# Performance work log

Hardware: AMD Instinct MI355X
Metric: run time of the kernel (lower is better)

The kernel has to match this reference:

```python
import jax, jax.numpy as jnp
import numpy as np

K = 7
SIGMA = 1.0
NUM_CLASSES = 17


def setup_inputs() -> dict:
    key = jax.random.key(0)
    k1, k2, k3 = jax.random.split(key, 3)
    B, C, N = 4, NUM_CLASSES, 4096
    logits = jax.random.normal(k1, (B, C, N), dtype=jnp.float32)
    labels = jax.random.randint(k2, (B, N), 0, NUM_CLASSES, dtype=jnp.int32)
    ins_T = jax.random.normal(k3, (B * N, NUM_CLASSES, NUM_CLASSES), dtype=jnp.float32)
    return {"logits": logits, "labels": labels, "ins_T": ins_T}


def reference(logits, labels, ins_T):
    B, C, N = logits.shape
    k = K
    x = jnp.transpose(logits, (0, 2, 1))  # [B, N, C]

    # Pairwise squared distances [B, N, N] and (k+1)-NN (smallest dists)
    sq = jnp.sum(x * x, axis=-1)  # [B, N]
    dists = sq[:, :, None] + sq[:, None, :] - 2.0 * jnp.einsum('bnc,bmc->bnm', x, x)
    _, idx = jax.lax.top_k(-dists, k + 1)  # smallest distances first
    idx = idx[:, :, 1:]  # drop self -> [B, N, k]

    flat = x.reshape(B * N, C)                 # [BN, C]
    labf = labels.reshape(-1)                  # [BN]
    idxf = (idx + jnp.arange(B)[:, None, None] * N).reshape(B * N, k)  # [BN, k]

    neigh_logits = flat[idxf]                          # [BN, k, C]
    neigh_labels = labf[idxf]                          # [BN, k]
    neigh_T = ins_T[idxf].reshape(B * N, k, -1)        # [BN, k, C*C]

    # distance map: +1 same label, -1 different, weighted by RBF affinity
    dmap = jnp.where(neigh_labels == labf[:, None], 1.0, -1.0)
    eij = jnp.exp(-jnp.sum((flat[:, None, :] - neigh_logits) ** 2, axis=2)
                  / (2.0 * SIGMA ** 2))
    dmap = jax.lax.stop_gradient(dmap * eij)  # detached in original

    T_dist = jnp.sum((ins_T.reshape(B * N, 1, -1) - neigh_T) ** 2, axis=2)  # [BN, k]
    return jnp.mean(dmap * T_dist)
```

## Files before the change

kernel.cpp:

```cpp
#include <hip/hip_runtime.h>

#define BB 4
#define CC 17
#define NN 4096
#define KN 7
#define NPTS (BB*NN)
#define PAIRS (NPTS*KN)
#define TT (CC*CC)
#define FINF 3.4e38f
#define RPB 64
#define SL 4
#define CSW 1024
#define NGRP 16
#define SCAP 48
#define SPAD 49
#define TDW 160
#define KNNBLKS ((NPTS/RPB)*SL)
#define TBLKS ((NPTS*TDW)/256)

typedef float f32x4 __attribute__((ext_vector_type(4)));
typedef short short8 __attribute__((ext_vector_type(8)));

__device__ __forceinline__ unsigned int rne_bf16(float x) {
    unsigned int u = __float_as_uint(x);
    return (u + 0x7FFFu + ((u >> 16) & 1u)) >> 16;
}

__device__ __forceinline__ bool lexless(float ad, int ai, float bd, int bi) {
    return (ad < bd) || (ad == bd && ai < bi);
}

__global__ __launch_bounds__(256) void prep_kernel(const float* __restrict__ logits,
                                                   float* __restrict__ xs,
                                                   unsigned short* __restrict__ xbA,
                                                   unsigned short* __restrict__ xbB,
                                                   float* __restrict__ sq,
                                                   unsigned int* __restrict__ zbuf) {
    if (blockIdx.x == 0) {
        for (int e = threadIdx.x; e < 768; e += 256) zbuf[e] = 0u;
    }
    int i = blockIdx.x * 256 + threadIdx.x;
    if (i >= NPTS) return;
    int b = i >> 12;
    int n = i & (NN - 1);
    const float* base = logits + (size_t)b * CC * NN + n;
    float v[24];
    float s = 0.f;
#pragma unroll
    for (int c = 0; c < CC; ++c) { v[c] = base[(size_t)c * NN]; s = fmaf(v[c], v[c], s); }
#pragma unroll
    for (int c = CC; c < 24; ++c) v[c] = 0.f;
    float4* dst = (float4*)(xs + (size_t)i * 24);
#pragma unroll
    for (int q = 0; q < 6; ++q)
        dst[q] = make_float4(v[4*q], v[4*q+1], v[4*q+2], v[4*q+3]);
    sq[i] = s;

    unsigned int w[16];
#pragma unroll
    for (int t = 0; t < 8; ++t)
        w[t] = rne_bf16(v[2*t]) | (rne_bf16(v[2*t+1]) << 16);
#pragma unroll
    for (int t = 9; t < 16; ++t) w[t] = 0u;
    w[8] = rne_bf16(v[16]) | (0x3F80u << 16);
    uint4* da = (uint4*)(xbA + (size_t)i * 32);
#pragma unroll
    for (int q = 0; q < 4; ++q)
        da[q] = make_uint4(w[4*q], w[4*q+1], w[4*q+2], w[4*q+3]);
    w[8] = rne_bf16(v[16]) | (rne_bf16(-0.5f * s) << 16);
    uint4* db = (uint4*)(xbB + (size_t)i * 24);
#pragma unroll
    for (int q = 0; q < 3; ++q)
        db[q] = make_uint4(w[4*q], w[4*q+1], w[4*q+2], w[4*q+3]);
}

#define INS4(T0, T1, T2, T3, R) {                       \
    float n0_ = fmaxf(T0, R); float s0_ = fminf(T0, R); \
    float n1_ = fmaxf(T1, s0_); float s1_ = fminf(T1, s0_); \
    float n2_ = fmaxf(T2, s1_); float s2_ = fminf(T2, s1_); \
    float n3_ = fmaxf(T3, s2_);                         \
    T0 = n0_; T1 = n1_; T2 = n2_; T3 = n3_; }

__global__ __launch_bounds__(256) void knn_kernel(const unsigned short* __restrict__ xbA,
                                                  const unsigned short* __restrict__ xbB,
                                                  const float* __restrict__ sq,
                                                  const float* __restrict__ xs,
                                                  const unsigned int* __restrict__ zbuf,
                                                  const float* __restrict__ insT,
                                                  unsigned int* __restrict__ Tb,
                                                  float* __restrict__ parts_d,
                                                  int* __restrict__ parts_i,
                                                  int doTb) {
    __shared__ int   scnt[RPB];
    __shared__ int   slist[RPB][SPAD];
    __shared__ float srank[RPB][SPAD];

    int bid = blockIdx.x;
    if (bid >= KNNBLKS) {
        int i = (bid - KNNBLKS) * 256 + threadIdx.x;
        int row = i / TDW;
        int dw  = i - row * TDW;
        int e   = dw * 2;
        const float* src = insT + (size_t)row * TT;
        float v0 = (e     < TT) ? src[e]     : 0.f;
        float v1 = (e + 1 < TT) ? src[e + 1] : 0.f;
        Tb[i] = rne_bf16(v0) | (rne_bf16(v1) << 16);
        return;
    }

    int tid   = threadIdx.x;
    int wid   = tid >> 6;
    int lane  = tid & 63;
    int grp4  = bid >> 2;
    int slice = bid & 3;
    int row0  = grp4 * RPB;
    int b     = row0 >> 12;
    int myrow = row0 + wid * 16;
    int cb    = b * NN + slice * CSW;
    int col   = lane & 15;
    int grp   = lane >> 4;
    int k0    = grp * 8;

    if (tid < RPB) scnt[tid] = 0;
    __syncthreads();

    short8 A = *reinterpret_cast<const short8*>(xbA + (size_t)(myrow + col) * 32 + k0);
    bool on = (grp < 3);
    const char* p = on ? ((const char*)xbB + (size_t)(cb + col) * 48 + grp * 16)
                       : (const char*)zbuf;
    long incv = on ? 3072 : 0;
    f32x4 z = {0.f, 0.f, 0.f, 0.f};

    float t0v[4], t1v[4], t2v[4], t3v[4];
#pragma unroll
    for (int j = 0; j < 4; ++j) { t0v[j] = -FINF; t1v[j] = -FINF; t2v[j] = -FINF; t3v[j] = -FINF; }

    unsigned int tb4 = 0;
#pragma unroll 2
    for (int g = 0; g < NGRP; ++g) {
        short8 b0 = *reinterpret_cast<const short8*>(p);
        short8 b1 = *reinterpret_cast<const short8*>(p + 768);
        short8 b2 = *reinterpret_cast<const short8*>(p + 1536);
        short8 b3 = *reinterpret_cast<const short8*>(p + 2304);
        p += incv;
        f32x4 a0 = __builtin_amdgcn_mfma_f32_16x16x32_bf16(A, b0, z, 0, 0, 0);
        f32x4 a1 = __builtin_amdgcn_mfma_f32_16x16x32_bf16(A, b1, z, 0, 0, 0);
        f32x4 a2 = __builtin_amdgcn_mfma_f32_16x16x32_bf16(A, b2, z, 0, 0, 0);
        f32x4 a3 = __builtin_amdgcn_mfma_f32_16x16x32_bf16(A, b3, z, 0, 0, 0);
#pragma unroll
        for (int j = 0; j < 4; ++j) {
            float r0 = __uint_as_float((__float_as_uint(a0[j]) & ~63u) | (tb4 + 0u));
            float r1 = __uint_as_float((__float_as_uint(a1[j]) & ~63u) | (tb4 + 1u));
            float r2 = __uint_as_float((__float_as_uint(a2[j]) & ~63u) | (tb4 + 2u));
            float r3 = __uint_as_float((__float_as_uint(a3[j]) & ~63u) | (tb4 + 3u));
            INS4(t0v[j], t1v[j], t2v[j], t3v[j], r0)
            INS4(t0v[j], t1v[j], t2v[j], t3v[j], r1)
            INS4(t0v[j], t1v[j], t2v[j], t3v[j], r2)
            INS4(t0v[j], t1v[j], t2v[j], t3v[j], r3)
        }
        tb4 += 4;
    }

    float ta[4];
#pragma unroll
    for (int j = 0; j < 4; ++j) {
        float v = t0v[j];
        int cnt = 0;
#pragma unroll
        for (int m = 1; m < 16; ++m) {
            float o = __shfl_xor(v, m);
            cnt += (o > v) ? 1 : 0;
        }
        float bv = (cnt <= 7) ? v : FINF;
        bv = fminf(bv, __shfl_xor(bv, 1));
        bv = fminf(bv, __shfl_xor(bv, 2));
        bv = fminf(bv, __shfl_xor(bv, 4));
        bv = fminf(bv, __shfl_xor(bv, 8));
        ta[j] = bv - (0.35f + 0.007f * fabsf(bv));
    }

#pragma unroll
    for (int j = 0; j < 4; ++j) {
        int rloc = wid * 16 + grp * 4 + j;
        float q0 = t0v[j], q1 = t1v[j], q2 = t2v[j], q3 = t3v[j];
        int nb = (q0 >= ta[j]) + (q1 >= ta[j]) + (q2 >= ta[j]) + (q3 >= ta[j]);
        if (nb) {
            int base = atomicAdd(&scnt[rloc], nb);
            if (base < SCAP)
                slist[rloc][base] = cb + (int)((__float_as_uint(q0) & 63u) << 4) + col;
            if (nb > 1 && base + 1 < SCAP)
                slist[rloc][base + 1] = cb + (int)((__float_as_uint(q1) & 63u) << 4) + col;
            if (nb > 2 && base + 2 < SCAP)
                slist[rloc][base + 2] = cb + (int)((__float_as_uint(q2) & 63u) << 4) + col;
            if (nb > 3 && base + 3 < SCAP)
                slist[rloc][base + 3] = cb + (int)((__float_as_uint(q3) & 63u) << 4) + col;
        }
    }
    __syncthreads();

    {
        int rowl = tid >> 2;
        int l4   = tid & 3;
        int rowg = row0 + rowl;
        int cnt  = scnt[rowl]; cnt = (cnt > SCAP) ? SCAP : cnt;
        const float4* qp = (const float4*)(xs + (size_t)rowg * 24);
        float qv[20];
#pragma unroll
        for (int c = 0; c < 5; ++c) {
            float4 t = qp[c];
            qv[4*c] = t.x; qv[4*c+1] = t.y; qv[4*c+2] = t.z; qv[4*c+3] = t.w;
        }
#pragma unroll
        for (int h = 0; h < 12; ++h) {
            int slot = l4 + 4 * h;
            if (slot < cnt) {
                int g = slist[rowl][slot];
                const float4* xp = (const float4*)(xs + (size_t)g * 24);
                float dot = 0.f;
#pragma unroll
                for (int c = 0; c < 5; ++c) {
                    float4 xv = xp[c];
                    dot = fmaf(qv[4*c+0], xv.x, dot);
                    dot = fmaf(qv[4*c+1], xv.y, dot);
                    dot = fmaf(qv[4*c+2], xv.z, dot);
                    dot = fmaf(qv[4*c+3], xv.w, dot);
                }
                srank[rowl][slot] = fmaf(-2.f, dot, sq[g]);
            }
        }
    }
    __syncthreads();

    if (tid < RPB) {
        int rowl = tid;
        int rowg = row0 + rowl;
        int cnt  = scnt[rowl]; cnt = (cnt > SCAP) ? SCAP : cnt;
        float bd[8]; int bi[8];
#pragma unroll
        for (int k = 0; k < 8; ++k) { bd[k] = FINF; bi[k] = 0x40000000 + (rowg << 3) + k; }
        for (int s = 0; s < cnt; ++s) {
            float r = srank[rowl][s];
            int   g = slist[rowl][s];
            if (lexless(r, g, bd[7], bi[7])) {
                bd[7] = r; bi[7] = g;
#pragma unroll
                for (int k = 7; k >= 1; --k) {
                    if (lexless(bd[k], bi[k], bd[k-1], bi[k-1])) {
                        float td = bd[k]; bd[k] = bd[k-1]; bd[k-1] = td;
                        int   ti = bi[k]; bi[k] = bi[k-1]; bi[k-1] = ti;
                    }
                }
            }
        }
        size_t ob = ((size_t)rowg * SL + slice) * 8;
#pragma unroll
        for (int k = 0; k < 8; ++k) { parts_d[ob + k] = bd[k]; parts_i[ob + k] = bi[k]; }
    }
}

__device__ __forceinline__ void merge32(int row, int lane,
                                        const float* __restrict__ parts_d,
                                        const int* __restrict__ parts_i,
                                        int* jn) {
    float d = FINF;
    int   gi = 0x50000000 + lane;
    if (lane < 32) {
        size_t ob = (size_t)row * 32 + lane;
        d  = parts_d[ob];
        gi = parts_i[ob];
        if (gi == row) d = FINF;
    }
#pragma unroll
    for (int r = 0; r < KN; ++r) {
        float g = d; int gj = gi;
#pragma unroll
        for (int off = 32; off >= 1; off >>= 1) {
            float od = __shfl_xor(g, off);
            int   oj = __shfl_xor(gj, off);
            if (lexless(od, oj, g, gj)) { g = od; gj = oj; }
        }
        jn[r] = gj;
        if (gi == gj) { d = FINF; gi = 0x58000000 + lane * 8 + r; }
    }
}

__global__ __launch_bounds__(256) void pairb_kernel(const float* __restrict__ xs,
                                                    const int* __restrict__ labels,
                                                    const unsigned int* __restrict__ Tb,
                                                    const float* __restrict__ parts_d,
                                                    const int* __restrict__ parts_i,
                                                    double* __restrict__ partials) {
    int wid  = threadIdx.x >> 6;
    int lane = threadIdx.x & 63;
    int bid  = blockIdx.x;
    int bswz = (bid & 7) * 512 + (bid >> 3);
    int row  = bswz * 4 + wid;
    int li   = labels[row];

    int jn[KN];
    merge32(row, lane, parts_d, parts_i, jn);

    const unsigned int* Ti = Tb + (size_t)row * TDW;
    unsigned int a0 = Ti[lane];
    unsigned int a1 = Ti[lane + 64];
    unsigned int a2 = (lane < 32) ? Ti[lane + 128] : 0u;
    float xi = (lane < 20) ? xs[(size_t)row * 24 + lane] : 0.f;

    unsigned int bv[KN][3];
    float xj[KN];
#pragma unroll
    for (int kk = 0; kk < KN; ++kk) {
        const unsigned int* Tj = Tb + (size_t)jn[kk] * TDW;
        bv[kk][0] = Tj[lane];
        bv[kk][1] = Tj[lane + 64];
        bv[kk][2] = (lane < 32) ? Tj[lane + 128] : 0u;
        xj[kk] = (lane < 20) ? xs[(size_t)jn[kk] * 24 + lane] : 0.f;
    }

    double acc = 0.0;
#pragma unroll
    for (int kk = 0; kk < KN; ++kk) {
        float td = 0.f;
        unsigned int aw[3] = {a0, a1, a2};
#pragma unroll
        for (int q = 0; q < 3; ++q) {
            unsigned int a = aw[q], bb = bv[kk][q];
            float dlo = __uint_as_float(a << 16)         - __uint_as_float(bb << 16);
            float dhi = __uint_as_float(a & 0xFFFF0000u) - __uint_as_float(bb & 0xFFFF0000u);
            td = fmaf(dlo, dlo, td);
            td = fmaf(dhi, dhi, td);
        }
        float df = xi - xj[kk];
        float dp = df * df;
#pragma unroll
        for (int off = 32; off >= 1; off >>= 1) {
            td += __shfl_xor(td, off);
            dp += __shfl_xor(dp, off);
        }
        if (lane == 0) {
            float eij = expf(-0.5f * dp);
            float sgn = (labels[jn[kk]] == li) ? eij : -eij;
            acc += (double)sgn * (double)td;
        }
    }
    __shared__ double wsum[4];
    if (lane == 0) wsum[wid] = acc;
    __syncthreads();
    if (threadIdx.x == 0)
        partials[blockIdx.x] = wsum[0] + wsum[1] + wsum[2] + wsum[3];
}

__global__ __launch_bounds__(256) void pair_f32_kernel(const float* __restrict__ xs,
                                                       const int* __restrict__ labels,
                                                       const float* __restrict__ insT,
                                                       const float* __restrict__ parts_d,
                                                       const int* __restrict__ parts_i,
                                                       double* __restrict__ partials) {
    int wid  = threadIdx.x >> 6;
    int lane = threadIdx.x & 63;
    int bid  = blockIdx.x;
    int bswz = (bid & 7) * 512 + (bid >> 3);
    int row  = bswz * 4 + wid;
    int li   = labels[row];

    int jn[KN];
    merge32(row, lane, parts_d, parts_i, jn);

    const float* Ti = insT + (size_t)row * TT;
    float tiv[5];
#pragma unroll
    for (int q = 0; q < 5; ++q) {
        int e = lane + 64 * q;
        tiv[q] = (e < TT) ? Ti[e] : 0.f;
    }
    float xi = (lane < 20) ? xs[(size_t)row * 24 + lane] : 0.f;
    double acc = 0.0;
#pragma unroll 1
    for (int kk = 0; kk < KN; ++kk) {
        int j = jn[kk];
        const float* Tj = insT + (size_t)j * TT;
        float td = 0.f;
#pragma unroll
        for (int q = 0; q < 5; ++q) {
            int e = lane + 64 * q;
            if (e < TT) { float df = tiv[q] - Tj[e]; td = fmaf(df, df, td); }
        }
        float dp = 0.f;
        if (lane < 20) { float df = xi - xs[(size_t)j * 24 + lane]; dp = df * df; }
#pragma unroll
        for (int off = 32; off >= 1; off >>= 1) {
            td += __shfl_xor(td, off);
            dp += __shfl_xor(dp, off);
        }
        if (lane == 0) {
            float eij = expf(-0.5f * dp);
            float sgn = (labels[j] == li) ? eij : -eij;
            acc += (double)sgn * (double)td;
        }
    }
    __shared__ double wsum[4];
    if (lane == 0) wsum[wid] = acc;
    __syncthreads();
    if (threadIdx.x == 0)
        partials[blockIdx.x] = wsum[0] + wsum[1] + wsum[2] + wsum[3];
}

__global__ __launch_bounds__(1024) void finalize_kernel(const double* __restrict__ partials,
                                                        int nparts, float* __restrict__ out) {
    __shared__ double red[1024];
    int t = threadIdx.x;
    double s = 0.0;
    for (int q = t; q < nparts; q += 1024) s += partials[q];
    red[t] = s;
    __syncthreads();
    for (int sft = 512; sft > 0; sft >>= 1) {
        if (t < sft) red[t] += red[t + sft];
        __syncthreads();
    }
    if (t == 0) out[0] = (float)(red[0] / (double)PAIRS);
}

extern "C" void kernel_launch(void* const* d_in, const int* in_sizes, int n_in,
                              void* d_out, int out_size, void* d_ws, size_t ws_size,
                              hipStream_t stream) {
    const float* logits = (const float*)d_in[0];
    const int*   labels = (const int*)d_in[1];
    const float* insT   = (const float*)d_in[2];
    float* out = (float*)d_out;

    const size_t o_part = 0;
    const size_t o_pd   = 32768;
    const size_t o_pi   = o_pd + 2097152;
    const size_t o_sq   = o_pi + 2097152;
    const size_t o_xs   = o_sq + 65536;
    const size_t o_xbA  = o_xs + 1572864;
    const size_t o_xbB  = o_xbA + 1048576;
    const size_t o_zb   = o_xbB + 786432;
    const size_t o_Tb   = o_zb + 4096;
    const size_t need_Tb = o_Tb + 10485760;

    char* ws = (char*)d_ws;
    double*         partials = (double*)(ws + o_part);
    float*          parts_d  = (float*)(ws + o_pd);
    int*            parts_i  = (int*)(ws + o_pi);
    float*          sq       = (float*)(ws + o_sq);
    float*          xs       = (float*)(ws + o_xs);
    unsigned short* xbA      = (unsigned short*)(ws + o_xbA);
    unsigned short* xbB      = (unsigned short*)(ws + o_xbB);
    unsigned int*   zbuf     = (unsigned int*)(ws + o_zb);
    unsigned int*   Tb       = (unsigned int*)(ws + o_Tb);

    bool useTb = (ws_size >= need_Tb);
    int knn_grid = KNNBLKS + (useTb ? TBLKS : 0);

    hipLaunchKernelGGL(prep_kernel, dim3(NPTS / 256), dim3(256), 0, stream,
                       logits, xs, xbA, xbB, sq, zbuf);
    hipLaunchKernelGGL(knn_kernel, dim3(knn_grid), dim3(256), 0, stream,
                       xbA, xbB, sq, xs, zbuf, insT, Tb, parts_d, parts_i, (int)useTb);
    if (useTb)
        hipLaunchKernelGGL(pairb_kernel, dim3(NPTS / 4), dim3(256), 0, stream,
                           xs, labels, Tb, parts_d, parts_i, partials);
    else
        hipLaunchKernelGGL(pair_f32_kernel, dim3(NPTS / 4), dim3(256), 0, stream,
                           xs, labels, insT, parts_d, parts_i, partials);
    hipLaunchKernelGGL(finalize_kernel, dim3(1), dim3(1024), 0, stream,
                       partials, NPTS / 4, out);
}
```

Baseline: 94.76 us.

## Move exact kNN rescoring from knn kernel into pair kernel wavefronts

The knn kernel no longer rescores candidates in shared memory and sorts them per row. It now writes surviving candidate indices per row and slice to a global list, using global atomic counters that the prep kernel zeroes. The pair kernel rescores up to 192 candidates per row in fp32, one candidate per lane, and picks the 7 nearest by wavefront shuffle reduction. The squared norm is stored inside xs, so the separate sq buffer goes away. This removes the block-level syncs and the serial single-thread insertion sort from knn, at the cost of global atomics and a larger candidate buffer in the workspace.

```diff
diff --git a/kernel.cpp b/kernel.cpp
--- a/kernel.cpp
+++ b/kernel.cpp
@@ -13,7 +13,6 @@
 #define CSW 1024
 #define NGRP 16
 #define SCAP 48
-#define SPAD 49
 #define TDW 160
 #define KNNBLKS ((NPTS/RPB)*SL)
 #define TBLKS ((NPTS*TDW)/256)
@@ -34,13 +33,16 @@
                                                    float* __restrict__ xs,
                                                    unsigned short* __restrict__ xbA,
                                                    unsigned short* __restrict__ xbB,
-                                                   float* __restrict__ sq,
-                                                   unsigned int* __restrict__ zbuf) {
+                                                   unsigned int* __restrict__ zbuf,
+                                                   int* __restrict__ gcnt) {
     if (blockIdx.x == 0) {
         for (int e = threadIdx.x; e < 768; e += 256) zbuf[e] = 0u;
     }
     int i = blockIdx.x * 256 + threadIdx.x;
     if (i >= NPTS) return;
+#pragma unroll
+    for (int q = 0; q < 4; ++q) gcnt[i * 4 + q] = 0;
+
     int b = i >> 12;
     int n = i & (NN - 1);
     const float* base = logits + (size_t)b * CC * NN + n;
@@ -50,28 +52,29 @@
     for (int c = 0; c < CC; ++c) { v[c] = base[(size_t)c * NN]; s = fmaf(v[c], v[c], s); }
 #pragma unroll
     for (int c = CC; c < 24; ++c) v[c] = 0.f;
+    v[20] = s;
     float4* dst = (float4*)(xs + (size_t)i * 24);
 #pragma unroll
     for (int q = 0; q < 6; ++q)
         dst[q] = make_float4(v[4*q], v[4*q+1], v[4*q+2], v[4*q+3]);
-    sq[i] = s;
-
-    unsigned int w[16];
+
+    unsigned int w[12];
 #pragma unroll
     for (int t = 0; t < 8; ++t)
         w[t] = rne_bf16(v[2*t]) | (rne_bf16(v[2*t+1]) << 16);
 #pragma unroll
-    for (int t = 9; t < 16; ++t) w[t] = 0u;
+    for (int t = 9; t < 12; ++t) w[t] = 0u;
     w[8] = rne_bf16(v[16]) | (0x3F80u << 16);
     uint4* da = (uint4*)(xbA + (size_t)i * 32);
-#pragma unroll
-    for (int q = 0; q < 4; ++q)
-        da[q] = make_uint4(w[4*q], w[4*q+1], w[4*q+2], w[4*q+3]);
+    da[0] = make_uint4(w[0], w[1], w[2], w[3]);
+    da[1] = make_uint4(w[4], w[5], w[6], w[7]);
+    da[2] = make_uint4(w[8], w[9], w[10], w[11]);
+    da[3] = make_uint4(0u, 0u, 0u, 0u);
     w[8] = rne_bf16(v[16]) | (rne_bf16(-0.5f * s) << 16);
     uint4* db = (uint4*)(xbB + (size_t)i * 24);
-#pragma unroll
-    for (int q = 0; q < 3; ++q)
-        db[q] = make_uint4(w[4*q], w[4*q+1], w[4*q+2], w[4*q+3]);
+    db[0] = make_uint4(w[0], w[1], w[2], w[3]);
+    db[1] = make_uint4(w[4], w[5], w[6], w[7]);
+    db[2] = make_uint4(w[8], w[9], w[10], w[11]);
 }
 
 #define INS4(T0, T1, T2, T3, R) {                       \
@@ -83,18 +86,12 @@
 
 __global__ __launch_bounds__(256) void knn_kernel(const unsigned short* __restrict__ xbA,
                                                   const unsigned short* __restrict__ xbB,
-                                                  const float* __restrict__ sq,
-                                                  const float* __restrict__ xs,
                                                   const unsigned int* __restrict__ zbuf,
                                                   const float* __restrict__ insT,
                                                   unsigned int* __restrict__ Tb,
-                                                  float* __restrict__ parts_d,
-                                                  int* __restrict__ parts_i,
+                                                  int* __restrict__ surv,
+                                                  int* __restrict__ gcnt,
                                                   int doTb) {
-    __shared__ int   scnt[RPB];
-    __shared__ int   slist[RPB][SPAD];
-    __shared__ float srank[RPB][SPAD];
-
     int bid = blockIdx.x;
     if (bid >= KNNBLKS) {
         int i = (bid - KNNBLKS) * 256 + threadIdx.x;
@@ -121,9 +118,6 @@
     int grp   = lane >> 4;
     int k0    = grp * 8;
 
-    if (tid < RPB) scnt[tid] = 0;
-    __syncthreads();
-
     short8 A = *reinterpret_cast<const short8*>(xbA + (size_t)(myrow + col) * 32 + k0);
     bool on = (grp < 3);
     const char* p = on ? ((const char*)xbB + (size_t)(cb + col) * 48 + grp * 16)
@@ -161,7 +155,6 @@
         tb4 += 4;
     }
 
-    float ta[4];
 #pragma unroll
     for (int j = 0; j < 4; ++j) {
         float v = t0v[j];
@@ -176,103 +169,73 @@
         bv = fminf(bv, __shfl_xor(bv, 2));
         bv = fminf(bv, __shfl_xor(bv, 4));
         bv = fminf(bv, __shfl_xor(bv, 8));
-        ta[j] = bv - (0.35f + 0.007f * fabsf(bv));
-    }
-
-#pragma unroll
-    for (int j = 0; j < 4; ++j) {
-        int rloc = wid * 16 + grp * 4 + j;
+        float ta = bv - (0.35f + 0.007f * fabsf(bv));
+
+        int rowg = row0 + wid * 16 + grp * 4 + j;
+        size_t gix = (size_t)rowg * SL + slice;
         float q0 = t0v[j], q1 = t1v[j], q2 = t2v[j], q3 = t3v[j];
-        int nb = (q0 >= ta[j]) + (q1 >= ta[j]) + (q2 >= ta[j]) + (q3 >= ta[j]);
+        int nb = (q0 >= ta) + (q1 >= ta) + (q2 >= ta) + (q3 >= ta);
         if (nb) {
-            int base = atomicAdd(&scnt[rloc], nb);
+            int base = atomicAdd(&gcnt[gix], nb);
             if (base < SCAP)
-                slist[rloc][base] = cb + (int)((__float_as_uint(q0) & 63u) << 4) + col;
+                surv[gix * SCAP + base] = cb + (int)((__float_as_uint(q0) & 63u) << 4) + col;
             if (nb > 1 && base + 1 < SCAP)
-                slist[rloc][base + 1] = cb + (int)((__float_as_uint(q1) & 63u) << 4) + col;
+                surv[gix * SCAP + base + 1] = cb + (int)((__float_as_uint(q1) & 63u) << 4) + col;
             if (nb > 2 && base + 2 < SCAP)
-                slist[rloc][base + 2] = cb + (int)((__float_as_uint(q2) & 63u) << 4) + col;
+                surv[gix * SCAP + base + 2] = cb + (int)((__float_as_uint(q2) & 63u) << 4) + col;
             if (nb > 3 && base + 3 < SCAP)
-                slist[rloc][base + 3] = cb + (int)((__float_as_uint(q3) & 63u) << 4) + col;
-        }
-    }
-    __syncthreads();
-
-    {
-        int rowl = tid >> 2;
-        int l4   = tid & 3;
-        int rowg = row0 + rowl;
-        int cnt  = scnt[rowl]; cnt = (cnt > SCAP) ? SCAP : cnt;
-        const float4* qp = (const float4*)(xs + (size_t)rowg * 24);
-        float qv[20];
-#pragma unroll
-        for (int c = 0; c < 5; ++c) {
-            float4 t = qp[c];
-            qv[4*c] = t.x; qv[4*c+1] = t.y; qv[4*c+2] = t.z; qv[4*c+3] = t.w;
-        }
-#pragma unroll
-        for (int h = 0; h < 12; ++h) {
-            int slot = l4 + 4 * h;
-            if (slot < cnt) {
-                int g = slist[rowl][slot];
-                const float4* xp = (const float4*)(xs + (size_t)g * 24);
-                float dot = 0.f;
-#pragma unroll
-                for (int c = 0; c < 5; ++c) {
-                    float4 xv = xp[c];
-                    dot = fmaf(qv[4*c+0], xv.x, dot);
-                    dot = fmaf(qv[4*c+1], xv.y, dot);
-                    dot = fmaf(qv[4*c+2], xv.z, dot);
-                    dot = fmaf(qv[4*c+3], xv.w, dot);
-                }
-                srank[rowl][slot] = fmaf(-2.f, dot, sq[g]);
+                surv[gix * SCAP + base + 3] = cb + (int)((__float_as_uint(q3) & 63u) << 4) + col;
+        }
+    }
+}
+
+__device__ __forceinline__ void select7(int row, int lane,
+                                        const int* __restrict__ surv,
+                                        const int* __restrict__ gcnt,
+                                        const float* __restrict__ xs,
+                                        int* jn) {
+    const float4* qp = (const float4*)(xs + (size_t)row * 24);
+    float qv[20];
+#pragma unroll
+    for (int c = 0; c < 5; ++c) {
+        float4 t = qp[c];
+        qv[4*c] = t.x; qv[4*c+1] = t.y; qv[4*c+2] = t.z; qv[4*c+3] = t.w;
+    }
+    float d0 = FINF, d1 = FINF, d2 = FINF;
+    int   g0 = 0x40000000 + lane * 4 + 0;
+    int   g1 = 0x40000000 + lane * 4 + 1;
+    int   g2 = 0x40000000 + lane * 4 + 2;
+#pragma unroll
+    for (int h = 0; h < 3; ++h) {
+        int slot = lane + 64 * h;
+        int sl   = slot / SCAP;
+        int k    = slot - sl * SCAP;
+        int cnt  = gcnt[row * SL + sl]; cnt = (cnt > SCAP) ? SCAP : cnt;
+        if (k < cnt) {
+            int gg = surv[((size_t)row * SL + sl) * SCAP + k];
+            const float4* xp = (const float4*)(xs + (size_t)gg * 24);
+            float dot = 0.f;
+#pragma unroll
+            for (int c = 0; c < 5; ++c) {
+                float4 xv = xp[c];
+                dot = fmaf(qv[4*c+0], xv.x, dot);
+                dot = fmaf(qv[4*c+1], xv.y, dot);
+                dot = fmaf(qv[4*c+2], xv.z, dot);
+                dot = fmaf(qv[4*c+3], xv.w, dot);
             }
-        }
-    }
-    __syncthreads();
-
-    if (tid < RPB) {
-        int rowl = tid;
-        int rowg = row0 + rowl;
-        int cnt  = scnt[rowl]; cnt = (cnt > SCAP) ? SCAP : cnt;
-        float bd[8]; int bi[8];
-#pragma unroll
-        for (int k = 0; k < 8; ++k) { bd[k] = FINF; bi[k] = 0x40000000 + (rowg << 3) + k; }
-        for (int s = 0; s < cnt; ++s) {
-            float r = srank[rowl][s];
-            int   g = slist[rowl][s];
-            if (lexless(r, g, bd[7], bi[7])) {
-                bd[7] = r; bi[7] = g;
-#pragma unroll
-                for (int k = 7; k >= 1; --k) {
-                    if (lexless(bd[k], bi[k], bd[k-1], bi[k-1])) {
-                        float td = bd[k]; bd[k] = bd[k-1]; bd[k-1] = td;
-                        int   ti = bi[k]; bi[k] = bi[k-1]; bi[k-1] = ti;
-                    }
-                }
-            }
-        }
-        size_t ob = ((size_t)rowg * SL + slice) * 8;
-#pragma unroll
-        for (int k = 0; k < 8; ++k) { parts_d[ob + k] = bd[k]; parts_i[ob + k] = bi[k]; }
-    }
-}
-
-__device__ __forceinline__ void merge32(int row, int lane,
-                                        const float* __restrict__ parts_d,
-                                        const int* __restrict__ parts_i,
-                                        int* jn) {
-    float d = FINF;
-    int   gi = 0x50000000 + lane;
-    if (lane < 32) {
-        size_t ob = (size_t)row * 32 + lane;
-        d  = parts_d[ob];
-        gi = parts_i[ob];
-        if (gi == row) d = FINF;
-    }
+            float r = fmaf(-2.f, dot, xs[(size_t)gg * 24 + 20]);
+            if (gg == row) r = FINF;
+            if (h == 0) { d0 = r; g0 = gg; }
+            else if (h == 1) { d1 = r; g1 = gg; }
+            else { d2 = r; g2 = gg; }
+        }
+    }
+    if (lexless(d1, g1, d0, g0)) { float t = d0; d0 = d1; d1 = t; int ti = g0; g0 = g1; g1 = ti; }
+    if (lexless(d2, g2, d1, g1)) { float t = d1; d1 = d2; d2 = t; int ti = g1; g1 = g2; g2 = ti; }
+    if (lexless(d1, g1, d0, g0)) { float t = d0; d0 = d1; d1 = t; int ti = g0; g0 = g1; g1 = ti; }
 #pragma unroll
     for (int r = 0; r < KN; ++r) {
-        float g = d; int gj = gi;
+        float g = d0; int gj = g0;
 #pragma unroll
         for (int off = 32; off >= 1; off >>= 1) {
             float od = __shfl_xor(g, off);
@@ -280,15 +243,19 @@
             if (lexless(od, oj, g, gj)) { g = od; gj = oj; }
         }
         jn[r] = gj;
-        if (gi == gj) { d = FINF; gi = 0x58000000 + lane * 8 + r; }
+        if (g0 == gj) {
+            d0 = d1; g0 = g1;
+            d1 = d2; g1 = g2;
+            d2 = FINF; g2 = 0x50000000 + lane * 8 + r;
+        }
     }
 }
 
 __global__ __launch_bounds__(256) void pairb_kernel(const float* __restrict__ xs,
                                                     const int* __restrict__ labels,
                                                     const unsigned int* __restrict__ Tb,
-                                                    const float* __restrict__ parts_d,
-                                                    const int* __restrict__ parts_i,
+                                                    const int* __restrict__ surv,
+                                                    const int* __restrict__ gcnt,
                                                     double* __restrict__ partials) {
     int wid  = threadIdx.x >> 6;
     int lane = threadIdx.x & 63;
@@ -298,7 +265,7 @@
     int li   = labels[row];
 
     int jn[KN];
-    merge32(row, lane, parts_d, parts_i, jn);
+    select7(row, lane, surv, gcnt, xs, jn);
 
     const unsigned int* Ti = Tb + (size_t)row * TDW;
     unsigned int a0 = Ti[lane];
@@ -353,8 +320,8 @@
 __global__ __launch_bounds__(256) void pair_f32_kernel(const float* __restrict__ xs,
                                                        const int* __restrict__ labels,
                                                        const float* __restrict__ insT,
-                                                       const float* __restrict__ parts_d,
-                                                       const int* __restrict__ parts_i,
+                                                       const int* __restrict__ surv,
+                                                       const int* __restrict__ gcnt,
                                                        double* __restrict__ partials) {
     int wid  = threadIdx.x >> 6;
     int lane = threadIdx.x & 63;
@@ -364,7 +331,7 @@
     int li   = labels[row];
 
     int jn[KN];
-    merge32(row, lane, parts_d, parts_i, jn);
+    select7(row, lane, surv, gcnt, xs, jn);
 
     const float* Ti = insT + (size_t)row * TT;
     float tiv[5];
@@ -429,10 +396,9 @@
     float* out = (float*)d_out;
 
     const size_t o_part = 0;
-    const size_t o_pd   = 32768;
-    const size_t o_pi   = o_pd + 2097152;
-    const size_t o_sq   = o_pi + 2097152;
-    const size_t o_xs   = o_sq + 65536;
+    const size_t o_gcnt = 32768;
+    const size_t o_surv = o_gcnt + 262144;
+    const size_t o_xs   = o_surv + 12582912;
     const size_t o_xbA  = o_xs + 1572864;
     const size_t o_xbB  = o_xbA + 1048576;
     const size_t o_zb   = o_xbB + 786432;
@@ -441,9 +407,8 @@
 
     char* ws = (char*)d_ws;
     double*         partials = (double*)(ws + o_part);
-    float*          parts_d  = (float*)(ws + o_pd);
-    int*            parts_i  = (int*)(ws + o_pi);
-    float*          sq       = (float*)(ws + o_sq);
+    int*            gcnt     = (int*)(ws + o_gcnt);
+    int*            surv     = (int*)(ws + o_surv);
     float*          xs       = (float*)(ws + o_xs);
     unsigned short* xbA      = (unsigned short*)(ws + o_xbA);
     unsigned short* xbB      = (unsigned short*)(ws + o_xbB);
@@ -454,15 +419,15 @@
     int knn_grid = KNNBLKS + (useTb ? TBLKS : 0);
 
     hipLaunchKernelGGL(prep_kernel, dim3(NPTS / 256), dim3(256), 0, stream,
-                       logits, xs, xbA, xbB, sq, zbuf);
+                       logits, xs, xbA, xbB, zbuf, gcnt);
     hipLaunchKernelGGL(knn_kernel, dim3(knn_grid), dim3(256), 0, stream,
-                       xbA, xbB, sq, xs, zbuf, insT, Tb, parts_d, parts_i, (int)useTb);
+                       xbA, xbB, zbuf, insT, Tb, surv, gcnt, (int)useTb);
     if (useTb)
         hipLaunchKernelGGL(pairb_kernel, dim3(NPTS / 4), dim3(256), 0, stream,
-                           xs, labels, Tb, parts_d, parts_i, partials);
+                           xs, labels, Tb, surv, gcnt, partials);
     else
         hipLaunchKernelGGL(pair_f32_kernel, dim3(NPTS / 4), dim3(256), 0, stream,
-                           xs, labels, insT, parts_d, parts_i, partials);
+                           xs, labels, insT, surv, gcnt, partials);
     hipLaunchKernelGGL(finalize_kernel, dim3(1), dim3(1024), 0, stream,
                        partials, NPTS / 4, out);
 }
```

Result: slower. 105.4 us (+11.3%).
